# Kernel tuning notes

Measured on AMD Instinct MI355X. Metric: run time of the kernel, lower is better.

## Reference

```python
import jax, jax.numpy as jnp
import numpy as np

N_TOKENS = 16384
INPUT_DIM = 4096
N_EXPERTS = 64
TOP_K = 8
EPS = 1e-12  # torch F.normalize eps
SCALE = 5.0


def l2_normalize(v):
    # matches torch.nn.functional.normalize(p=2, dim=-1, eps=1e-12)
    norm = jnp.sqrt(jnp.sum(v * v, axis=-1, keepdims=True))
    return v / jnp.maximum(norm, EPS)


def setup_inputs() -> dict:
    key = jax.random.key(0)
    kx, ks = jax.random.split(key)
    x = jax.random.normal(kx, (N_TOKENS, INPUT_DIM), dtype=jnp.float32)
    # signatures are L2-normalized in the module (_normalize_signatures)
    sig = jax.random.normal(ks, (N_EXPERTS, INPUT_DIM), dtype=jnp.float32)
    phase_signatures = l2_normalize(sig)
    return {"x": x, "phase_signatures": phase_signatures}


def reference(x, phase_signatures):
    x_norm = l2_normalize(x)                                   # [N, D]
    resonance = jnp.einsum('nd,ed->ne', x_norm, phase_signatures)  # [N, E]
    resonance = resonance * SCALE
    k = min(TOP_K, resonance.shape[-1])
    top_k_resonance, top_k_indices = jax.lax.top_k(resonance, k)   # [N, k]
    weights = jax.nn.softplus(top_k_resonance)                 # [N, k]
    return (weights, top_k_indices, resonance)
```

## Files before the change

### kernel.cpp

```cpp
#include <hip/hip_runtime.h>
#include <cmath>


#define N_TOKENS 16384
#define DIM      4096
#define NE       64
#define TOPK     8
#define SCALE    5.0f
#define EPS      1e-12f
#define NSLAB    32

typedef short  frag   __attribute__((ext_vector_type(8)));
typedef float  f32x16 __attribute__((ext_vector_type(16)));
typedef int    i32x4  __attribute__((ext_vector_type(4)));

__device__ __forceinline__ void split3(float v, unsigned& h1, unsigned& h2, unsigned& h3) {
    unsigned u  = __builtin_bit_cast(unsigned, v);
    unsigned r1 = (u + 0x7FFFu + ((u >> 16) & 1u)) & 0xFFFF0000u;
    float    d1 = v - __builtin_bit_cast(float, r1);
    unsigned w  = __builtin_bit_cast(unsigned, d1);
    unsigned r2 = (w + 0x7FFFu + ((w >> 16) & 1u)) & 0xFFFF0000u;
    float    d2 = d1 - __builtin_bit_cast(float, r2);
    unsigned z  = __builtin_bit_cast(unsigned, d2);
    unsigned r3 = (z + 0x7FFFu + ((z >> 16) & 1u)) & 0xFFFF0000u;
    h1 = r1 >> 16; h2 = r2 >> 16; h3 = r3 >> 16;
}

__launch_bounds__(256)
__global__ void convert_sig(const float* __restrict__ sig,
                            short* __restrict__ h1,
                            short* __restrict__ h2,
                            short* __restrict__ h3) {
    const int tid  = blockIdx.x * 256 + threadIdx.x;
    const int lane = tid & 63;
    const int kb   = (tid >> 6) & 255;
    const int tile = tid >> 14;
    const int e31  = lane & 31, hf = lane >> 5;
    const float* src = sig + (size_t)(tile * 32 + e31) * DIM + kb * 16 + hf * 8;
    const float4 v0 = *(const float4*)(src);
    const float4 v1 = *(const float4*)(src + 4);
    const float vs[8] = {v0.x, v0.y, v0.z, v0.w, v1.x, v1.y, v1.z, v1.w};
    frag o1, o2, o3;
#pragma unroll
    for (int p = 0; p < 8; ++p) {
        unsigned a, b, c;
        split3(vs[p], a, b, c);
        o1[p] = (short)a; o2[p] = (short)b; o3[p] = (short)c;
    }
    const int base = ((tile * 256 + kb) * 64 + lane) * 8;
    *(frag*)(h1 + base) = o1;
    *(frag*)(h2 + base) = o2;
    *(frag*)(h3 + base) = o3;
}

__device__ __forceinline__ void stage_slab(const float* __restrict__ x, int tb,
                                           int c0, float* slabbuf, int w, int lane) {
    const int i1 = w * 64 + lane;
    const int r1 = i1 >> 5;
    const int j1 = (i1 & 31) ^ (r1 & 7);
    const float* g1 = x + (size_t)(tb + r1) * DIM + c0 + 4 * j1;
    const int i2 = i1 + 512;
    const int r2 = i2 >> 5;
    const int j2 = (i2 & 31) ^ (r2 & 7);
    const float* g2 = x + (size_t)(tb + r2) * DIM + c0 + 4 * j2;
    float* l1 = slabbuf + w * 256;
    float* l2 = slabbuf + w * 256 + 2048;
    __builtin_amdgcn_global_load_lds(
        (const __attribute__((address_space(1))) void*)g1,
        (__attribute__((address_space(3))) void*)l1, 16, 0, 0);
    __builtin_amdgcn_global_load_lds(
        (const __attribute__((address_space(1))) void*)g2,
        (__attribute__((address_space(3))) void*)l2, 16, 0, 0);
}

__launch_bounds__(512, 4)
__global__ void gemm_fused(const float* __restrict__ x,
                           const short* __restrict__ sh1,
                           const short* __restrict__ sh2,
                           const short* __restrict__ sh3,
                           float* __restrict__ outR,
                           float* __restrict__ outW,
                           float* __restrict__ outI) {
    __shared__ __align__(16) char smem[45056];
    float* slab = (float*)smem;
    float (*red)[64][34] = (float(*)[64][34])smem;
    float (*res)[68]     = (float(*)[68])(smem + 34816);
    float (*sqred)[32]   = (float(*)[32])(smem + 43520);
    float* scl           = (float*)(smem + 44544);

    const int t    = threadIdx.x;
    const int lane = t & 63;
    const int w    = t >> 6;
    const int l31  = lane & 31;
    const int half = lane >> 5;

    const int tb = blockIdx.x * 32;

    const short* b1p = sh1 + ((size_t)(w * 64) + lane) * 8;
    const short* b2p = sh2 + ((size_t)(w * 64) + lane) * 8;
    const short* b3p = sh3 + ((size_t)(w * 64) + lane) * 8;
    const int TILE1 = 256 * 64 * 8;

    f32x16 c0 = {};
    f32x16 c1 = {};
    float sq = 0.f;

    const int kk = 4 * w + 2 * half;
    const int rr = l31;
    const int roff = rr * 128;
    const int sl0 = (kk ^ (rr & 7)) * 4;
    const int sl1 = ((kk + 1) ^ (rr & 7)) * 4;

    stage_slab(x, tb, 0, slab, w, lane);
    __syncthreads();

#pragma unroll 1
    for (int s = 0; s < NSLAB; ++s) {
        const int b = s & 1;
        if (s + 1 < NSLAB)
            stage_slab(x, tb, (s + 1) * 128, slab + (1 - b) * 4096, w, lane);

        const frag b1a = *(const frag*)(b1p);
        const frag b1b = *(const frag*)(b1p + TILE1);
        const frag b2a = *(const frag*)(b2p);
        const frag b2b = *(const frag*)(b2p + TILE1);
        const frag b3a = *(const frag*)(b3p);
        const frag b3b = *(const frag*)(b3p + TILE1);

        const float* base = slab + b * 4096 + roff;
        const float4 va = *(const float4*)(base + sl0);
        const float4 vb = *(const float4*)(base + sl1);

        const float vals[8] = {va.x, va.y, va.z, va.w, vb.x, vb.y, vb.z, vb.w};
        i32x4 a1i, a2i, a3i;
#pragma unroll
        for (int p = 0; p < 4; ++p) {
            const float v0 = vals[2 * p], v1 = vals[2 * p + 1];
            sq = fmaf(v0, v0, sq);
            sq = fmaf(v1, v1, sq);
            unsigned h10, h20, h30, h11, h21, h31;
            split3(v0, h10, h20, h30);
            split3(v1, h11, h21, h31);
            a1i[p] = (int)(h10 | (h11 << 16));
            a2i[p] = (int)(h20 | (h21 << 16));
            a3i[p] = (int)(h30 | (h31 << 16));
        }
        const frag A1 = __builtin_bit_cast(frag, a1i);
        const frag A2 = __builtin_bit_cast(frag, a2i);
        const frag A3 = __builtin_bit_cast(frag, a3i);

        c0 = __builtin_amdgcn_mfma_f32_32x32x16_bf16(A1, b1a, c0, 0, 0, 0);
        c1 = __builtin_amdgcn_mfma_f32_32x32x16_bf16(A1, b1b, c1, 0, 0, 0);
        c0 = __builtin_amdgcn_mfma_f32_32x32x16_bf16(A1, b2a, c0, 0, 0, 0);
        c1 = __builtin_amdgcn_mfma_f32_32x32x16_bf16(A1, b2b, c1, 0, 0, 0);
        c0 = __builtin_amdgcn_mfma_f32_32x32x16_bf16(A2, b1a, c0, 0, 0, 0);
        c1 = __builtin_amdgcn_mfma_f32_32x32x16_bf16(A2, b1b, c1, 0, 0, 0);
        c0 = __builtin_amdgcn_mfma_f32_32x32x16_bf16(A1, b3a, c0, 0, 0, 0);
        c1 = __builtin_amdgcn_mfma_f32_32x32x16_bf16(A1, b3b, c1, 0, 0, 0);
        c0 = __builtin_amdgcn_mfma_f32_32x32x16_bf16(A3, b1a, c0, 0, 0, 0);
        c1 = __builtin_amdgcn_mfma_f32_32x32x16_bf16(A3, b1b, c1, 0, 0, 0);
        c0 = __builtin_amdgcn_mfma_f32_32x32x16_bf16(A2, b2a, c0, 0, 0, 0);
        c1 = __builtin_amdgcn_mfma_f32_32x32x16_bf16(A2, b2b, c1, 0, 0, 0);

        b1p += 4096; b2p += 4096; b3p += 4096;
        __syncthreads();
    }

    sq += __shfl_xor(sq, 32);
    if (lane < 32) sqred[w][l31] = sq;

    if (w >= 4) {
#pragma unroll
        for (int r = 0; r < 16; ++r) {
            red[w - 4][lane][r]      = c0[r];
            red[w - 4][lane][16 + r] = c1[r];
        }
    }
    __syncthreads();

    if (t < 32) {
        float q = 0.f;
#pragma unroll
        for (int ww = 0; ww < 8; ++ww) q += sqred[ww][t];
        scl[t] = SCALE / fmaxf(sqrtf(q), EPS);
    }

    if (w < 4) {
#pragma unroll
        for (int r = 0; r < 16; ++r) {
            red[w][lane][r]      = c0[r] + red[w][lane][r];
            red[w][lane][16 + r] = c1[r] + red[w][lane][16 + r];
        }
    }
    __syncthreads();

    const int wm = w & 3, tile = w >> 2;
    const int et = l31 + 32 * tile;
#pragma unroll
    for (int j = 0; j < 4; ++j) {
        const int R = 4 * w + j;
        const float a = red[0][lane][R] + red[1][lane][R] +
                        red[2][lane][R] + red[3][lane][R];
        const int token = j + 8 * wm + 4 * half;
        res[token][et] = a * scl[token];
    }
    __syncthreads();

    {
        const int token = t >> 4, q4 = (t & 15) * 4;
        *(float4*)(outR + (size_t)(tb + token) * NE + q4) =
            *(const float4*)(&res[token][q4]);
    }

#pragma unroll 1
    for (int tt = 0; tt < 4; ++tt) {
        const int token = 4 * w + tt;
        const float v = res[token][lane];
        const unsigned u = __builtin_bit_cast(unsigned, v);
        const unsigned sbits = u ^ ((unsigned)(((int)u) >> 31) | 0x80000000u);
        unsigned long long cur = ((unsigned long long)sbits << 32) | (unsigned)(63 - lane);

        float bw = 0.f;
        int   bi = 0;
#pragma unroll
        for (int m = 0; m < TOPK; ++m) {
            unsigned long long r = cur;
#pragma unroll
            for (int d = 32; d >= 1; d >>= 1) {
                const unsigned long long o = __shfl_xor(r, d);
                r = (o > r) ? o : r;
            }
            const int we = 63 - (int)(r & 63ull);
            const float bv = __shfl(v, we);
            if (lane == we) cur = 0ull;
            if (lane == m) { bw = bv; bi = we; }
        }
        if (lane < TOPK) {
            const size_t ob = (size_t)(tb + token) * TOPK + lane;
            outW[ob] = log1pf(expf(bw));
            outI[ob] = (float)bi;
        }
    }
}

extern "C" void kernel_launch(void* const* d_in, const int* in_sizes, int n_in,
                              void* d_out, int out_size, void* d_ws, size_t ws_size,
                              hipStream_t stream) {
    const float* x   = (const float*)d_in[0];
    const float* sig = (const float*)d_in[1];
    float* out  = (float*)d_out;
    float* outW = out;
    float* outI = out + (size_t)N_TOKENS * TOPK;
    float* outR = out + (size_t)N_TOKENS * TOPK * 2;

    const size_t SIGE = (size_t)NE * DIM;
    short* sh1 = (short*)d_ws;
    short* sh2 = sh1 + SIGE;
    short* sh3 = sh2 + SIGE;

    convert_sig<<<128, 256, 0, stream>>>(sig, sh1, sh2, sh3);
    gemm_fused<<<N_TOKENS / 32, 512, 0, stream>>>(x, sh1, sh2, sh3, outR, outW, outI);
}
```

Before: 386.4 us.

## Triple-buffer x slabs with prefetch distance two and cheapen bf16 splitting

The x slab staging moves from double to triple buffering in LDS, prefetching two slabs ahead. The full __syncthreads is replaced by an explicit s_waitcnt vmcnt(2) plus s_barrier, so the newest async global-to-LDS load can stay in flight across the barrier. The three-way bf16 split also drops round-to-nearest-even in favour of a simple +0x8000 round, and truncates the third piece instead of rounding it. This cuts VALU work in both the conversion and the GEMM loop, at some cost in split accuracy and LDS size (now 48KB).

```diff
diff --git a/kernel.cpp b/kernel.cpp
--- a/kernel.cpp
+++ b/kernel.cpp
@@ -14,16 +14,14 @@
 typedef float  f32x16 __attribute__((ext_vector_type(16)));
 typedef int    i32x4  __attribute__((ext_vector_type(4)));
 
-__device__ __forceinline__ void split3(float v, unsigned& h1, unsigned& h2, unsigned& h3) {
+__device__ __forceinline__ void split3c(float v, unsigned& r1, unsigned& r2, unsigned& z) {
     unsigned u  = __builtin_bit_cast(unsigned, v);
-    unsigned r1 = (u + 0x7FFFu + ((u >> 16) & 1u)) & 0xFFFF0000u;
-    float    d1 = v - __builtin_bit_cast(float, r1);
-    unsigned w  = __builtin_bit_cast(unsigned, d1);
-    unsigned r2 = (w + 0x7FFFu + ((w >> 16) & 1u)) & 0xFFFF0000u;
-    float    d2 = d1 - __builtin_bit_cast(float, r2);
-    unsigned z  = __builtin_bit_cast(unsigned, d2);
-    unsigned r3 = (z + 0x7FFFu + ((z >> 16) & 1u)) & 0xFFFF0000u;
-    h1 = r1 >> 16; h2 = r2 >> 16; h3 = r3 >> 16;
+    r1 = (u + 0x8000u) & 0xFFFF0000u;
+    float d1 = v - __builtin_bit_cast(float, r1);
+    unsigned w = __builtin_bit_cast(unsigned, d1);
+    r2 = (w + 0x8000u) & 0xFFFF0000u;
+    float d2 = d1 - __builtin_bit_cast(float, r2);
+    z  = __builtin_bit_cast(unsigned, d2);
 }
 
 __launch_bounds__(256)
@@ -44,8 +42,8 @@
 #pragma unroll
     for (int p = 0; p < 8; ++p) {
         unsigned a, b, c;
-        split3(vs[p], a, b, c);
-        o1[p] = (short)a; o2[p] = (short)b; o3[p] = (short)c;
+        split3c(vs[p], a, b, c);
+        o1[p] = (short)(a >> 16); o2[p] = (short)(b >> 16); o3[p] = (short)(c >> 16);
     }
     const int base = ((tile * 256 + kb) * 64 + lane) * 8;
     *(frag*)(h1 + base) = o1;
@@ -53,24 +51,19 @@
     *(frag*)(h3 + base) = o3;
 }
 
-__device__ __forceinline__ void stage_slab(const float* __restrict__ x, int tb,
-                                           int c0, float* slabbuf, int w, int lane) {
-    const int i1 = w * 64 + lane;
-    const int r1 = i1 >> 5;
-    const int j1 = (i1 & 31) ^ (r1 & 7);
-    const float* g1 = x + (size_t)(tb + r1) * DIM + c0 + 4 * j1;
-    const int i2 = i1 + 512;
-    const int r2 = i2 >> 5;
-    const int j2 = (i2 & 31) ^ (r2 & 7);
-    const float* g2 = x + (size_t)(tb + r2) * DIM + c0 + 4 * j2;
-    float* l1 = slabbuf + w * 256;
-    float* l2 = slabbuf + w * 256 + 2048;
-    __builtin_amdgcn_global_load_lds(
-        (const __attribute__((address_space(1))) void*)g1,
-        (__attribute__((address_space(3))) void*)l1, 16, 0, 0);
-    __builtin_amdgcn_global_load_lds(
-        (const __attribute__((address_space(1))) void*)g2,
-        (__attribute__((address_space(3))) void*)l2, 16, 0, 0);
+__device__ __forceinline__ void stage_slab128(const float* __restrict__ x, int tb,
+                                              int kcol, float* dst, int w, int lane) {
+#pragma unroll
+    for (int cc = 0; cc < 2; ++cc) {
+        const int i = cc * 512 + w * 64 + lane;
+        const int r = i >> 5;
+        const int j = (i & 31) ^ (r & 7);
+        const float* g = x + (size_t)(tb + r) * DIM + kcol + 4 * j;
+        float* l = dst + (size_t)(cc * 512 + w * 64) * 4;
+        __builtin_amdgcn_global_load_lds(
+            (const __attribute__((address_space(1))) void*)g,
+            (__attribute__((address_space(3))) void*)l, 16, 0, 0);
+    }
 }
 
 __launch_bounds__(512, 4)
@@ -81,7 +74,7 @@
                            float* __restrict__ outR,
                            float* __restrict__ outW,
                            float* __restrict__ outI) {
-    __shared__ __align__(16) char smem[45056];
+    __shared__ __align__(16) char smem[49152];
     float* slab = (float*)smem;
     float (*red)[64][34] = (float(*)[64][34])smem;
     float (*res)[68]     = (float(*)[68])(smem + 34816);
@@ -95,31 +88,33 @@
     const int half = lane >> 5;
 
     const int tb = blockIdx.x * 32;
+    const int TILE1 = 256 * 64 * 8;
+    const int SLABB = 8 * 64 * 8;
 
     const short* b1p = sh1 + ((size_t)(w * 64) + lane) * 8;
     const short* b2p = sh2 + ((size_t)(w * 64) + lane) * 8;
     const short* b3p = sh3 + ((size_t)(w * 64) + lane) * 8;
-    const int TILE1 = 256 * 64 * 8;
+
+    const int rr = l31;
+    const int sw = rr & 7;
+    const int roff = rr * 128;
+    const int cA = 4 * w + 2 * half;
 
     f32x16 c0 = {};
     f32x16 c1 = {};
     float sq = 0.f;
 
-    const int kk = 4 * w + 2 * half;
-    const int rr = l31;
-    const int roff = rr * 128;
-    const int sl0 = (kk ^ (rr & 7)) * 4;
-    const int sl1 = ((kk + 1) ^ (rr & 7)) * 4;
-
-    stage_slab(x, tb, 0, slab, w, lane);
-    __syncthreads();
-
+    stage_slab128(x, tb, 0, slab, w, lane);
+    stage_slab128(x, tb, 128, slab + 4096, w, lane);
+    __builtin_amdgcn_sched_barrier(0);
+    asm volatile("s_waitcnt vmcnt(2)" ::: "memory");
+    __builtin_amdgcn_sched_barrier(0);
+    __builtin_amdgcn_s_barrier();
+    __builtin_amdgcn_sched_barrier(0);
+
+    int bcur = 0;
 #pragma unroll 1
     for (int s = 0; s < NSLAB; ++s) {
-        const int b = s & 1;
-        if (s + 1 < NSLAB)
-            stage_slab(x, tb, (s + 1) * 128, slab + (1 - b) * 4096, w, lane);
-
         const frag b1a = *(const frag*)(b1p);
         const frag b1b = *(const frag*)(b1p + TILE1);
         const frag b2a = *(const frag*)(b2p);
@@ -127,9 +122,14 @@
         const frag b3a = *(const frag*)(b3p);
         const frag b3b = *(const frag*)(b3p + TILE1);
 
-        const float* base = slab + b * 4096 + roff;
-        const float4 va = *(const float4*)(base + sl0);
-        const float4 vb = *(const float4*)(base + sl1);
+        if (s < NSLAB - 2) {
+            int bnxt = bcur + 2; if (bnxt >= 3) bnxt -= 3;
+            stage_slab128(x, tb, (s + 2) * 128, slab + bnxt * 4096, w, lane);
+        }
+
+        const float* base = slab + bcur * 4096 + roff;
+        const float4 va = *(const float4*)(base + ((cA ^ sw) << 2));
+        const float4 vb = *(const float4*)(base + (((cA + 1) ^ sw) << 2));
 
         const float vals[8] = {va.x, va.y, va.z, va.w, vb.x, vb.y, vb.z, vb.w};
         i32x4 a1i, a2i, a3i;
@@ -138,12 +138,12 @@
             const float v0 = vals[2 * p], v1 = vals[2 * p + 1];
             sq = fmaf(v0, v0, sq);
             sq = fmaf(v1, v1, sq);
-            unsigned h10, h20, h30, h11, h21, h31;
-            split3(v0, h10, h20, h30);
-            split3(v1, h11, h21, h31);
-            a1i[p] = (int)(h10 | (h11 << 16));
-            a2i[p] = (int)(h20 | (h21 << 16));
-            a3i[p] = (int)(h30 | (h31 << 16));
+            unsigned r10_, r20_, z0_, r11_, r21_, z1_;
+            split3c(v0, r10_, r20_, z0_);
+            split3c(v1, r11_, r21_, z1_);
+            a1i[p] = (int)((r10_ >> 16) | (r11_ & 0xFFFF0000u));
+            a2i[p] = (int)((r20_ >> 16) | (r21_ & 0xFFFF0000u));
+            a3i[p] = (int)((z0_  >> 16) | (z1_  & 0xFFFF0000u));
         }
         const frag A1 = __builtin_bit_cast(frag, a1i);
         const frag A2 = __builtin_bit_cast(frag, a2i);
@@ -162,8 +162,14 @@
         c0 = __builtin_amdgcn_mfma_f32_32x32x16_bf16(A2, b2a, c0, 0, 0, 0);
         c1 = __builtin_amdgcn_mfma_f32_32x32x16_bf16(A2, b2b, c1, 0, 0, 0);
 
-        b1p += 4096; b2p += 4096; b3p += 4096;
-        __syncthreads();
+        __builtin_amdgcn_sched_barrier(0);
+        asm volatile("s_waitcnt vmcnt(2)" ::: "memory");
+        __builtin_amdgcn_sched_barrier(0);
+        __builtin_amdgcn_s_barrier();
+        __builtin_amdgcn_sched_barrier(0);
+
+        b1p += SLABB; b2p += SLABB; b3p += SLABB;
+        if (++bcur == 3) bcur = 0;
     }
 
     sq += __shfl_xor(sq, 32);
```

Result: no change. 391.1 us (+1.2%).
